# Optimization experiments

Hardware: AMD Instinct MI355X
Metric: run time of the kernel (lower is better)

## Reference

```python
import jax, jax.numpy as jnp
import numpy as np

B, S, D = 8, 4096, 768
HEADS = 12
NEIGHBORS = 2
DILATION = 1
KERNEL = 1 + 2 * NEIGHBORS  # 5
DIM_HEAD = D // HEADS


def setup_inputs() -> dict:
    key = jax.random.key(0)
    ks = jax.random.split(key, 11)
    sc = 1.0 / np.sqrt(D)
    return {
        "x": jax.random.normal(ks[0], (B, S, D), dtype=jnp.float32),
        "Wq": jax.random.normal(ks[1], (D, D), dtype=jnp.float32) * sc,
        "bq": jax.random.normal(ks[2], (D,), dtype=jnp.float32) * 0.02,
        "Wk": jax.random.normal(ks[3], (D, D), dtype=jnp.float32) * sc,
        "bk": jax.random.normal(ks[4], (D,), dtype=jnp.float32) * 0.02,
        "Wv": jax.random.normal(ks[5], (D, D), dtype=jnp.float32) * sc,
        "bv": jax.random.normal(ks[6], (D,), dtype=jnp.float32) * 0.02,
        "Wo": jax.random.normal(ks[7], (D, D), dtype=jnp.float32) * sc,
        "bo": jax.random.normal(ks[8], (D,), dtype=jnp.float32) * 0.02,
        "gamma": jnp.ones((D,), dtype=jnp.float32),
        "beta": jnp.zeros((D,), dtype=jnp.float32),
    }


def _extract_seq_patches(x, kernel_size, dilation):
    # [B, S, D] -> [B, S, kernel_size, D] of dilated local windows, zero-padded.
    seq_len = x.shape[1]
    patch_size = kernel_size + (dilation - 1) * (kernel_size - 1)
    pad_r = (patch_size - 1) // 2
    pad_l = patch_size - pad_r - 1
    xp = jnp.pad(x, ((0, 0), (pad_l, pad_r), (0, 0)))
    # small fixed loop over kernel positions (kernel_size = 5)
    return jnp.stack([xp[:, i:i + seq_len] for i in range(0, patch_size, dilation)], axis=2)


def reference(x, Wq, bq, Wk, bk, Wv, bv, Wo, bo, gamma, beta):
    patches = _extract_seq_patches(x, KERNEL, DILATION)  # [B, S, K, D]
    q = x @ Wq + bq                                       # [B, S, D]
    k = patches @ Wk + bk                                 # [B, S, K, D]
    v = patches @ Wv + bv                                 # [B, S, K, D]
    # split heads
    q = q.reshape(B, S, HEADS, DIM_HEAD)
    k = k.reshape(B, S, KERNEL, HEADS, DIM_HEAD)
    v = v.reshape(B, S, KERNEL, HEADS, DIM_HEAD)
    scale = jnp.sqrt(jnp.asarray(DIM_HEAD, dtype=q.dtype))
    scores = jnp.einsum('bshd,bskhd->bshk', q, k) / scale  # [B, S, H, K]
    p = jax.nn.softmax(scores, axis=-1)
    att = jnp.einsum('bshk,bskhd->bshd', p, v)             # [B, S, H, dh]
    att = att.reshape(B, S, D)
    att = att @ Wo + bo
    y = att + x
    # LayerNorm over last dim
    mu = jnp.mean(y, axis=-1, keepdims=True)
    var = jnp.var(y, axis=-1, keepdims=True)
    y = (y - mu) / jnp.sqrt(var + 1e-5) * gamma + beta
    return y
```

## Files before the change

### kernel.cpp

```cpp
#include <hip/hip_runtime.h>

#define B_  8
#define S_  4096
#define D_  768
#define H_  12
#define M_  (B_ * S_)
#define NQKV_ 2304
#define NTILES 12

typedef unsigned short u16;
typedef __attribute__((ext_vector_type(4))) float  f32x4;
typedef __attribute__((ext_vector_type(8))) __bf16 bf16x8;
typedef __attribute__((ext_vector_type(4))) u16    u16x4;

#define GAS __attribute__((address_space(1)))
#define LAS __attribute__((address_space(3)))

__device__ __forceinline__ u16 f2bf(float f) {
    unsigned u = __float_as_uint(f);
    u += 0x7FFF + ((u >> 16) & 1);
    return (u16)(u >> 16);
}
__device__ __forceinline__ float bf2f(u16 h) {
    return __uint_as_float(((unsigned)h) << 16);
}

__device__ __forceinline__ void gload_lds16(const void* g, void* l) {
    __builtin_amdgcn_global_load_lds((const GAS void*)g, (LAS void*)l, 16, 0, 0);
}

__device__ __forceinline__ int xcd_swz(int bid, int nwg) {
    return (bid & 7) * (nwg >> 3) + (bid >> 3);
}

__global__ __launch_bounds__(256) void castx_kernel(const float* __restrict__ x,
                                                    u16* __restrict__ xb) {
    const int i = blockIdx.x * 256 + threadIdx.x;
    const float4 v = ((const float4*)x)[i];
    u16x4 o;
    o.x = f2bf(v.x); o.y = f2bf(v.y); o.z = f2bf(v.z); o.w = f2bf(v.w);
    ((u16x4*)xb)[i] = o;
}

__global__ __launch_bounds__(256) void wtrans_kernel(const float* __restrict__ Wq,
                                                     const float* __restrict__ Wk,
                                                     const float* __restrict__ Wv,
                                                     const float* __restrict__ Wo,
                                                     u16* __restrict__ Wb) {
    const float* W = (blockIdx.z == 0) ? Wq : (blockIdx.z == 1) ? Wk
                   : (blockIdx.z == 2) ? Wv : Wo;
    u16* O = Wb + (size_t)blockIdx.z * D_ * D_;
    __shared__ float tile[32][33];
    const int tx = threadIdx.x & 31, ty = threadIdx.x >> 5;
    const int k0 = blockIdx.y * 32, n0 = blockIdx.x * 32;
#pragma unroll
    for (int j = 0; j < 4; j++)
        tile[ty + j * 8][tx] = W[(size_t)(k0 + ty + j * 8) * D_ + n0 + tx];
    __syncthreads();
#pragma unroll
    for (int j = 0; j < 4; j++)
        O[(size_t)(n0 + ty + j * 8) * D_ + k0 + tx] = f2bf(tile[tx][ty + j * 8]);
}


#define MFMA16(AF, BF)                                                       \
    __builtin_amdgcn_s_setprio(1);                                           \
    _Pragma("unroll") for (int mi = 0; mi < 4; ++mi)                         \
        _Pragma("unroll") for (int ni = 0; ni < 4; ++ni)                     \
            acc[mi][ni] = __builtin_amdgcn_mfma_f32_16x16x32_bf16(           \
                AF[mi], BF[ni], acc[mi][ni], 0, 0, 0);                       \
    __builtin_amdgcn_s_setprio(0)

#define RD(p, imm) (*(const bf16x8*)((p) + (imm)))

template <int MODE>
__global__ __launch_bounds__(256, 2) void gemm2_kernel(
    const u16* __restrict__ A, const u16* __restrict__ Wb,
    const float* __restrict__ b0, const float* __restrict__ b1,
    const float* __restrict__ b2,
    u16* __restrict__ outb, const u16* __restrict__ xres) {
    extern __shared__ char lds[];

    const int t = threadIdx.x;
    const int w = t >> 6, l = t & 63;
    const int wm = w >> 1, wn = w & 1;

    const int NTN = (MODE == 0) ? 18 : 6;
    const int work = xcd_swz(blockIdx.x, gridDim.x);
    const int mt = work / NTN, nt = work % NTN;
    const int m0 = mt * 128;
    const int col0 = nt * 128;
    const int widx = (MODE == 0) ? (nt / 6) : 3;
    const int n0w  = (MODE == 0) ? (nt % 6) * 128 : col0;

    const int srow = w * 32 + (l >> 3);
    const int schunk = (l & 7) ^ ((l >> 3) & 7);
    const u16* Asrc = A + (size_t)(m0 + srow) * D_ + schunk * 8;
    const u16* Bsrc = Wb + (size_t)widx * (D_ * D_)
                         + (size_t)(n0w + srow) * D_ + schunk * 8;
    char* const dstA = lds + w * 4096;
    char* const dstB = lds + 16384 + w * 4096;

    const int ck0 = (((l >> 4) ^ (l & 7)) << 4);
    const int ck1 = ((((l >> 4) + 4) ^ (l & 7)) << 4);
    const char* aB = lds + (wm * 64 + (l & 15)) * 128;
    const char* bB = lds + 16384 + (wn * 64 + (l & 15)) * 128;

    f32x4 acc[4][4];
#pragma unroll
    for (int i = 0; i < 4; i++)
#pragma unroll
        for (int j = 0; j < 4; j++) acc[i][j] = (f32x4){0.f, 0.f, 0.f, 0.f};

    auto STAGE = [&](int tk, int b) {
        const int ko = tk * 64;
        char* da = dstA + b * 32768;
        char* db = dstB + b * 32768;
#pragma unroll
        for (int g = 0; g < 4; ++g) {
            gload_lds16(Asrc + ko + g * 8 * D_, da + g * 1024);
            gload_lds16(Bsrc + ko + g * 8 * D_, db + g * 1024);
        }
    };

    STAGE(0, 0);
    __syncthreads();

#pragma unroll
    for (int X = 0; X < NTILES; ++X) {
        const int cb = (X & 1) * 32768;
        if (X + 1 < NTILES) STAGE(X + 1, (X & 1) ^ 1);

        bf16x8 af[4], bf[4];
#pragma unroll
        for (int mi = 0; mi < 4; ++mi) af[mi] = RD(aB, cb + mi * 2048 + ck0);
#pragma unroll
        for (int ni = 0; ni < 4; ++ni) bf[ni] = RD(bB, cb + ni * 2048 + ck0);
        MFMA16(af, bf);
#pragma unroll
        for (int mi = 0; mi < 4; ++mi) af[mi] = RD(aB, cb + mi * 2048 + ck1);
#pragma unroll
        for (int ni = 0; ni < 4; ++ni) bf[ni] = RD(bB, cb + ni * 2048 + ck1);
        MFMA16(af, bf);

        __syncthreads();
    }

    const int crow0 = m0 + wm * 64 + ((l >> 4) << 2);
    const int ccol0 = col0 + wn * 64 + (l & 15);
    if (MODE == 0) {
        const float* bias = (widx == 0) ? b0 : (widx == 1) ? b1 : b2;
        const int bcol0 = ccol0 - widx * D_;
#pragma unroll
        for (int mi = 0; mi < 4; ++mi)
#pragma unroll
            for (int ni = 0; ni < 4; ++ni) {
                const float bv = bias[bcol0 + ni * 16];
#pragma unroll
                for (int r = 0; r < 4; ++r)
                    outb[(size_t)(crow0 + mi * 16 + r) * NQKV_ + ccol0 + ni * 16] =
                        f2bf(acc[mi][ni][r] + bv);
            }
    } else {
#pragma unroll
        for (int mi = 0; mi < 4; ++mi)
#pragma unroll
            for (int ni = 0; ni < 4; ++ni) {
                const int col = ccol0 + ni * 16;
                const float bv = b0[col];
#pragma unroll
                for (int r = 0; r < 4; ++r) {
                    const size_t idx = (size_t)(crow0 + mi * 16 + r) * D_ + col;
                    outb[idx] = f2bf(acc[mi][ni][r] + bv + bf2f(xres[idx]));
                }
            }
    }
}

__global__ __launch_bounds__(256) void attn_kernel(const u16* __restrict__ QKV,
                                                   const float* __restrict__ bk,
                                                   const float* __restrict__ bv,
                                                   u16* __restrict__ att) {
    const int gw = xcd_swz(blockIdx.x, gridDim.x) * 4 + (threadIdx.x >> 6);
    const int l  = threadIdx.x & 63;
    const int hq = gw % 3;
    const int m  = gw / 3;
    const int s  = m & (S_ - 1);
    const int col = hq * 256 + l * 4;
    const u16* base = QKV + (size_t)m * NQKV_;

    const u16x4 qv = *(const u16x4*)(base + col);
    float qf[4];
#pragma unroll
    for (int j = 0; j < 4; j++) qf[j] = bf2f(qv[j]);

    float sc[5];
#pragma unroll
    for (int i = 0; i < 5; i++) {
        const int sp = s + i - 2;
        float p;
        if (sp >= 0 && sp < S_) {
            const u16x4 kv = *(const u16x4*)(base + (i - 2) * NQKV_ + D_ + col);
            p = qf[0] * bf2f(kv[0]) + qf[1] * bf2f(kv[1])
              + qf[2] * bf2f(kv[2]) + qf[3] * bf2f(kv[3]);
        } else {
            const float4 kb = *(const float4*)(bk + col);
            p = qf[0] * kb.x + qf[1] * kb.y + qf[2] * kb.z + qf[3] * kb.w;
        }
#pragma unroll
        for (int off = 1; off < 16; off <<= 1) p += __shfl_xor(p, off, 64);
        sc[i] = p * 0.125f;
    }
    float mx = sc[0];
#pragma unroll
    for (int i = 1; i < 5; i++) mx = fmaxf(mx, sc[i]);
    float e[5], sum = 0.f;
#pragma unroll
    for (int i = 0; i < 5; i++) { e[i] = __expf(sc[i] - mx); sum += e[i]; }
    const float inv = 1.f / sum;

    float o[4] = {0.f, 0.f, 0.f, 0.f};
#pragma unroll
    for (int i = 0; i < 5; i++) {
        const float wgt = e[i] * inv;
        const int sp = s + i - 2;
        if (sp >= 0 && sp < S_) {
            const u16x4 vv = *(const u16x4*)(base + (i - 2) * NQKV_ + 2 * D_ + col);
#pragma unroll
            for (int j = 0; j < 4; j++) o[j] += wgt * bf2f(vv[j]);
        } else {
            const float4 vb = *(const float4*)(bv + col);
            o[0] += wgt * vb.x; o[1] += wgt * vb.y;
            o[2] += wgt * vb.z; o[3] += wgt * vb.w;
        }
    }
    u16x4 ov;
#pragma unroll
    for (int j = 0; j < 4; j++) ov[j] = f2bf(o[j]);
    *(u16x4*)(att + (size_t)m * D_ + col) = ov;
}

__global__ __launch_bounds__(256) void ln_kernel(const u16* __restrict__ Yb,
                                                 const float* __restrict__ gamma,
                                                 const float* __restrict__ beta,
                                                 float* __restrict__ out) {
    const int w = threadIdx.x >> 6, l = threadIdx.x & 63;
    const int row = blockIdx.x * 4 + w;
    const u16* r = Yb + (size_t)row * D_;
    const int c0 = l * 4;

    float v[3][4];
    float s = 0.f, s2 = 0.f;
#pragma unroll
    for (int c = 0; c < 3; ++c) {
        const u16x4 hv = *(const u16x4*)(r + c * 256 + c0);
#pragma unroll
        for (int j = 0; j < 4; ++j) {
            const float f = bf2f(hv[j]);
            v[c][j] = f;
            s += f;
            s2 += f * f;
        }
    }
#pragma unroll
    for (int off = 1; off < 64; off <<= 1) {
        s  += __shfl_xor(s,  off, 64);
        s2 += __shfl_xor(s2, off, 64);
    }
    const float mu  = s * (1.f / 768.f);
    const float var = s2 * (1.f / 768.f) - mu * mu;
    const float inv = rsqrtf(var + 1e-5f);

    float* o = out + (size_t)row * D_;
#pragma unroll
    for (int c = 0; c < 3; ++c) {
        const float4 g = *(const float4*)(gamma + c * 256 + c0);
        const float4 b = *(const float4*)(beta  + c * 256 + c0);
        float4 ov;
        ov.x = (v[c][0] - mu) * inv * g.x + b.x;
        ov.y = (v[c][1] - mu) * inv * g.y + b.y;
        ov.z = (v[c][2] - mu) * inv * g.z + b.z;
        ov.w = (v[c][3] - mu) * inv * g.w + b.w;
        *(float4*)(o + c * 256 + c0) = ov;
    }
}

extern "C" void kernel_launch(void* const* d_in, const int* in_sizes, int n_in,
                              void* d_out, int out_size, void* d_ws, size_t ws_size,
                              hipStream_t stream) {
    const float* x     = (const float*)d_in[0];
    const float* Wq    = (const float*)d_in[1];
    const float* bq    = (const float*)d_in[2];
    const float* Wk    = (const float*)d_in[3];
    const float* bk    = (const float*)d_in[4];
    const float* Wv    = (const float*)d_in[5];
    const float* bv    = (const float*)d_in[6];
    const float* Wo    = (const float*)d_in[7];
    const float* bo    = (const float*)d_in[8];
    const float* gamma = (const float*)d_in[9];
    const float* beta  = (const float*)d_in[10];

    char* ws = (char*)d_ws;
    u16*   Wb  = (u16*)ws;
    u16*   xb  = (u16*)(ws + 4718592);
    u16*   QKV = (u16*)(ws + 4718592 + 50331648);
    u16*   yb  = QKV;
    u16*   att = (u16*)d_out;

    (void)hipFuncSetAttribute(reinterpret_cast<const void*>(&gemm2_kernel<0>),
                              hipFuncAttributeMaxDynamicSharedMemorySize, 65536);
    (void)hipFuncSetAttribute(reinterpret_cast<const void*>(&gemm2_kernel<1>),
                              hipFuncAttributeMaxDynamicSharedMemorySize, 65536);

    castx_kernel<<<(M_ * D_) / (256 * 4), 256, 0, stream>>>(x, xb);
    wtrans_kernel<<<dim3(24, 24, 4), 256, 0, stream>>>(Wq, Wk, Wv, Wo, Wb);
    gemm2_kernel<0><<<(M_ / 128) * 18, 256, 65536, stream>>>(xb, Wb, bq, bk, bv,
                                                             QKV, nullptr);
    attn_kernel<<<(M_ * 3) / 4, 256, 0, stream>>>(QKV, bk, bv, att);
    gemm2_kernel<1><<<(M_ / 128) * 6, 256, 65536, stream>>>(att, Wb, bo, nullptr, nullptr,
                                                            yb, xb);
    ln_kernel<<<M_ / 4, 256, 0, stream>>>(yb, gamma, beta, (float*)d_out);
}
```

Measured before the change: 289.7 us.

## Load GEMM B operand directly from global into registers, halve LDS

The GEMM kernel no longer stages the weight tile through LDS. Each wave loads its B fragments straight from global memory into a double-buffered register array one K-tile ahead, and only the A tile stays in LDS, which shrinks shared memory from 64KB dynamic to 32KB static. This is meant to cut LDS traffic and raise occupancy, at the cost of more VGPRs for the prefetched fragments and uncoalesced-ish 16B global loads of weights that are now read redundantly by the two waves sharing a column.

New measurement: 434.5 us. 50.0% more time.

```diff
diff --git a/kernel.cpp b/kernel.cpp
--- a/kernel.cpp
+++ b/kernel.cpp
@@ -63,13 +63,19 @@
 }
 
 
-#define MFMA16(AF, BF)                                                       \
+#define MFMA8K(AF, BS, KH)                                                   \
     __builtin_amdgcn_s_setprio(1);                                           \
     _Pragma("unroll") for (int mi = 0; mi < 4; ++mi)                         \
         _Pragma("unroll") for (int ni = 0; ni < 4; ++ni)                     \
             acc[mi][ni] = __builtin_amdgcn_mfma_f32_16x16x32_bf16(           \
-                AF[mi], BF[ni], acc[mi][ni], 0, 0, 0);                       \
+                AF[mi], BS[ni][KH], acc[mi][ni], 0, 0, 0);                   \
     __builtin_amdgcn_s_setprio(0)
+
+#define LOAD_B(SEL, kt)                                                      \
+    _Pragma("unroll") for (int ni = 0; ni < 4; ++ni)                         \
+        _Pragma("unroll") for (int kh = 0; kh < 2; ++kh)                     \
+            B2[SEL][ni][kh] = *(const bf16x8*)(Bp + (size_t)ni * 16 * D_     \
+                                               + (kt) * 64 + kh * 32)
 
 #define RD(p, imm) (*(const bf16x8*)((p) + (imm)))
 
@@ -79,7 +85,7 @@
     const float* __restrict__ b0, const float* __restrict__ b1,
     const float* __restrict__ b2,
     u16* __restrict__ outb, const u16* __restrict__ xres) {
-    extern __shared__ char lds[];
+    __shared__ char lds[32768];
 
     const int t = threadIdx.x;
     const int w = t >> 6, l = t & 63;
@@ -96,15 +102,16 @@
     const int srow = w * 32 + (l >> 3);
     const int schunk = (l & 7) ^ ((l >> 3) & 7);
     const u16* Asrc = A + (size_t)(m0 + srow) * D_ + schunk * 8;
-    const u16* Bsrc = Wb + (size_t)widx * (D_ * D_)
-                         + (size_t)(n0w + srow) * D_ + schunk * 8;
     char* const dstA = lds + w * 4096;
-    char* const dstB = lds + 16384 + w * 4096;
-
-    const int ck0 = (((l >> 4) ^ (l & 7)) << 4);
-    const int ck1 = ((((l >> 4) + 4) ^ (l & 7)) << 4);
-    const char* aB = lds + (wm * 64 + (l & 15)) * 128;
-    const char* bB = lds + 16384 + (wn * 64 + (l & 15)) * 128;
+
+    const int fr = l & 15;
+    const int kg = l >> 4;
+    const int ck0 = ((kg ^ (l & 7)) << 4);
+    const int ck1 = (((kg + 4) ^ (l & 7)) << 4);
+    const char* aB = lds + (wm * 64 + fr) * 128;
+
+    const u16* Bp = Wb + (size_t)widx * (D_ * D_)
+                       + (size_t)(n0w + wn * 64 + fr) * D_ + kg * 8;
 
     f32x4 acc[4][4];
 #pragma unroll
@@ -112,42 +119,41 @@
 #pragma unroll
         for (int j = 0; j < 4; j++) acc[i][j] = (f32x4){0.f, 0.f, 0.f, 0.f};
 
-    auto STAGE = [&](int tk, int b) {
+    bf16x8 B2[2][4][2];
+
+    auto STAGE_A = [&](int tk, int b) {
         const int ko = tk * 64;
-        char* da = dstA + b * 32768;
-        char* db = dstB + b * 32768;
-#pragma unroll
-        for (int g = 0; g < 4; ++g) {
+        char* da = dstA + b * 16384;
+#pragma unroll
+        for (int g = 0; g < 4; ++g)
             gload_lds16(Asrc + ko + g * 8 * D_, da + g * 1024);
-            gload_lds16(Bsrc + ko + g * 8 * D_, db + g * 1024);
+    };
+
+    STAGE_A(0, 0);
+    LOAD_B(0, 0);
+    __syncthreads();
+
+#pragma unroll
+    for (int X = 0; X < NTILES; ++X) {
+        const int cb = (X & 1) * 16384;
+        if (X + 1 < NTILES) {
+            STAGE_A(X + 1, (X & 1) ^ 1);
+            LOAD_B((X + 1) & 1, X + 1);
         }
-    };
-
-    STAGE(0, 0);
-    __syncthreads();
-
-#pragma unroll
-    for (int X = 0; X < NTILES; ++X) {
-        const int cb = (X & 1) * 32768;
-        if (X + 1 < NTILES) STAGE(X + 1, (X & 1) ^ 1);
-
-        bf16x8 af[4], bf[4];
+
+        bf16x8 af[4];
 #pragma unroll
         for (int mi = 0; mi < 4; ++mi) af[mi] = RD(aB, cb + mi * 2048 + ck0);
-#pragma unroll
-        for (int ni = 0; ni < 4; ++ni) bf[ni] = RD(bB, cb + ni * 2048 + ck0);
-        MFMA16(af, bf);
+        MFMA8K(af, B2[X & 1], 0);
 #pragma unroll
         for (int mi = 0; mi < 4; ++mi) af[mi] = RD(aB, cb + mi * 2048 + ck1);
-#pragma unroll
-        for (int ni = 0; ni < 4; ++ni) bf[ni] = RD(bB, cb + ni * 2048 + ck1);
-        MFMA16(af, bf);
+        MFMA8K(af, B2[X & 1], 1);
 
         __syncthreads();
     }
 
-    const int crow0 = m0 + wm * 64 + ((l >> 4) << 2);
-    const int ccol0 = col0 + wn * 64 + (l & 15);
+    const int crow0 = m0 + wm * 64 + (kg << 2);
+    const int ccol0 = col0 + wn * 64 + fr;
     if (MODE == 0) {
         const float* bias = (widx == 0) ? b0 : (widx == 1) ? b1 : b2;
         const int bcol0 = ccol0 - widx * D_;
@@ -307,17 +313,12 @@
     u16*   yb  = QKV;
     u16*   att = (u16*)d_out;
 
-    (void)hipFuncSetAttribute(reinterpret_cast<const void*>(&gemm2_kernel<0>),
-                              hipFuncAttributeMaxDynamicSharedMemorySize, 65536);
-    (void)hipFuncSetAttribute(reinterpret_cast<const void*>(&gemm2_kernel<1>),
-                              hipFuncAttributeMaxDynamicSharedMemorySize, 65536);
-
     castx_kernel<<<(M_ * D_) / (256 * 4), 256, 0, stream>>>(x, xb);
     wtrans_kernel<<<dim3(24, 24, 4), 256, 0, stream>>>(Wq, Wk, Wv, Wo, Wb);
-    gemm2_kernel<0><<<(M_ / 128) * 18, 256, 65536, stream>>>(xb, Wb, bq, bk, bv,
-                                                             QKV, nullptr);
+    gemm2_kernel<0><<<(M_ / 128) * 18, 256, 0, stream>>>(xb, Wb, bq, bk, bv,
+                                                         QKV, nullptr);
     attn_kernel<<<(M_ * 3) / 4, 256, 0, stream>>>(QKV, bk, bv, att);
-    gemm2_kernel<1><<<(M_ / 128) * 6, 256, 65536, stream>>>(att, Wb, bo, nullptr, nullptr,
-                                                            yb, xb);
+    gemm2_kernel<1><<<(M_ / 128) * 6, 256, 0, stream>>>(att, Wb, bo, nullptr, nullptr,
+                                                        yb, xb);
     ln_kernel<<<M_ / 4, 256, 0, stream>>>(yb, gamma, beta, (float*)d_out);
 }
```
